# Kernel tuning notes

Hardware: AMD Instinct MI355X
Metric: run time of the kernel (lower is better)

## Reference

```python
import jax, jax.numpy as jnp
import numpy as np

WINDOW_SIZE = 11
CHANNELS = 3
SIGMA = 1.5


def _gaussian_window():
    # 1D gaussian, normalized, then outer product -> [C,1,K,K] depthwise kernel
    x = np.arange(WINDOW_SIZE) - WINDOW_SIZE // 2
    g = np.exp(-(x.astype(np.float32) ** 2) / (2.0 * SIGMA ** 2))
    g = g / g.sum()
    w2d = np.outer(g, g).astype(np.float32)
    w = np.broadcast_to(w2d[None, None], (CHANNELS, 1, WINDOW_SIZE, WINDOW_SIZE))
    return jnp.asarray(np.ascontiguousarray(w))


def _dwconv(x, w):
    # depthwise conv, SAME padding (pad = K//2), NCHW / OIHW layout
    pad = WINDOW_SIZE // 2
    return jax.lax.conv_general_dilated(
        x, w,
        window_strides=(1, 1),
        padding=[(pad, pad), (pad, pad)],
        dimension_numbers=("NCHW", "OIHW", "NCHW"),
        feature_group_count=CHANNELS,
    )


def setup_inputs() -> dict:
    key = jax.random.key(0)
    k1, k2 = jax.random.split(key)
    shape = (32, 3, 512, 512)
    img1 = jax.random.normal(k1, shape, dtype=jnp.float32)
    img2 = jax.random.normal(k2, shape, dtype=jnp.float32)
    return {"img1": img1, "img2": img2}


def reference(img1, img2):
    w = _gaussian_window().astype(img1.dtype)
    x1 = (img1 + 1.0) * 0.5
    x2 = (img2 + 1.0) * 0.5

    mu1 = _dwconv(x1, w)
    mu2 = _dwconv(x2, w)
    mu1_sq = mu1 * mu1
    mu2_sq = mu2 * mu2
    mu1_mu2 = mu1 * mu2

    sigma1_sq = _dwconv(x1 * x1, w) - mu1_sq
    sigma2_sq = _dwconv(x2 * x2, w) - mu2_sq
    sigma12 = _dwconv(x1 * x2, w) - mu1_mu2

    C1 = 0.01 ** 2
    C2 = 0.03 ** 2
    ssim_map = ((2.0 * mu1_mu2 + C1) * (2.0 * sigma12 + C2)) / (
        (mu1_sq + mu2_sq + C1) * (sigma1_sq + sigma2_sq + C2)
    )
    return 1.0 - jnp.mean(ssim_map)
```

## Files before the change

kernel.cpp:

```cpp
#include <hip/hip_runtime.h>
#include <cmath>

#define KW    11
#define PADW  5
#define BX    64
#define BY    32
#define TR    (BY + 2*PADW)
#define HST   68
#define IMG   512
#define NPIX  25165824.0

struct GaussW { float g[6]; };

__global__ __launch_bounds__(256, 2)
void ssim_main(const float* __restrict__ img1, const float* __restrict__ img2,
               double* __restrict__ acc, GaussW gw) {
  __shared__ float hb[5][TR][HST];
  __shared__ float red[4];

  const int tid = threadIdx.x;
  const int x0 = (blockIdx.x & 7) * BX;
  const int y0 = (blockIdx.x >> 3) * BY;
  const size_t plane = (size_t)blockIdx.y * (IMG * IMG);
  const float* base1 = img1 + plane;
  const float* base2 = img2 + plane;

  for (int t = tid; t < TR * 8; t += 256) {
    const int r = t >> 3;
    const int g = t & 7;
    const int gy = y0 - PADW + r;
    const int xb = x0 + 8 * g - 8;
    const bool rowok = ((unsigned)gy < (unsigned)IMG);

    float a[24], b[24];
    #pragma unroll
    for (int i = 0; i < 6; i++) {
      const int cb = xb + 4 * i;
      if (rowok && ((unsigned)cb < (unsigned)IMG)) {
        const float4 v1 = *(const float4*)(base1 + (size_t)gy * IMG + cb);
        const float4 v2 = *(const float4*)(base2 + (size_t)gy * IMG + cb);
        a[4*i+0] = fmaf(v1.x, 0.5f, 0.5f);  b[4*i+0] = fmaf(v2.x, 0.5f, 0.5f);
        a[4*i+1] = fmaf(v1.y, 0.5f, 0.5f);  b[4*i+1] = fmaf(v2.y, 0.5f, 0.5f);
        a[4*i+2] = fmaf(v1.z, 0.5f, 0.5f);  b[4*i+2] = fmaf(v2.z, 0.5f, 0.5f);
        a[4*i+3] = fmaf(v1.w, 0.5f, 0.5f);  b[4*i+3] = fmaf(v2.w, 0.5f, 0.5f);
      } else {
        a[4*i+0] = 0.f; a[4*i+1] = 0.f; a[4*i+2] = 0.f; a[4*i+3] = 0.f;
        b[4*i+0] = 0.f; b[4*i+1] = 0.f; b[4*i+2] = 0.f; b[4*i+3] = 0.f;
      }
    }

    float p11[18], p22[18], p12[18];
    #pragma unroll
    for (int i = 0; i < 18; i++) {
      const float u = a[i + 3], v = b[i + 3];
      p11[i] = u * u; p22[i] = v * v; p12[i] = u * v;
    }

    float c0[8], c1[8], c2[8], c3[8], c4[8];
    #pragma unroll
    for (int j = 0; j < 8; j++) { c0[j]=0.f; c1[j]=0.f; c2[j]=0.f; c3[j]=0.f; c4[j]=0.f; }
    #pragma unroll
    for (int k = 0; k < KW; k++) {
      const float gk = gw.g[(k < 6) ? k : 10 - k];
      #pragma unroll
      for (int j = 0; j < 8; j++) {
        c0[j] = fmaf(gk, a[j + 3 + k], c0[j]);
        c1[j] = fmaf(gk, b[j + 3 + k], c1[j]);
        c2[j] = fmaf(gk, p11[j + k], c2[j]);
        c3[j] = fmaf(gk, p22[j + k], c3[j]);
        c4[j] = fmaf(gk, p12[j + k], c4[j]);
      }
    }

    const int col = 8 * g;
    *(float4*)&hb[0][r][col]     = make_float4(c0[0], c0[1], c0[2], c0[3]);
    *(float4*)&hb[0][r][col + 4] = make_float4(c0[4], c0[5], c0[6], c0[7]);
    *(float4*)&hb[1][r][col]     = make_float4(c1[0], c1[1], c1[2], c1[3]);
    *(float4*)&hb[1][r][col + 4] = make_float4(c1[4], c1[5], c1[6], c1[7]);
    *(float4*)&hb[2][r][col]     = make_float4(c2[0], c2[1], c2[2], c2[3]);
    *(float4*)&hb[2][r][col + 4] = make_float4(c2[4], c2[5], c2[6], c2[7]);
    *(float4*)&hb[3][r][col]     = make_float4(c3[0], c3[1], c3[2], c3[3]);
    *(float4*)&hb[3][r][col + 4] = make_float4(c3[4], c3[5], c3[6], c3[7]);
    *(float4*)&hb[4][r][col]     = make_float4(c4[0], c4[1], c4[2], c4[3]);
    *(float4*)&hb[4][r][col + 4] = make_float4(c4[4], c4[5], c4[6], c4[7]);
  }

  __syncthreads();

  const int w = tid >> 6;
  const int c = tid & 63;
  const int ys = 8 * w;

  const float C1 = (float)(0.01 * 0.01);
  const float C2 = (float)(0.03 * 0.03);

  float win[5][11];
  #pragma unroll
  for (int t = 0; t < 10; t++) {
    #pragma unroll
    for (int q = 0; q < 5; q++) win[q][t] = hb[q][ys + t][c];
  }

  float accs = 0.f;
  #pragma unroll
  for (int i = 0; i < 8; i++) {
    #pragma unroll
    for (int q = 0; q < 5; q++) win[q][(10 + i) % 11] = hb[q][ys + 10 + i][c];

    float vb[5];
    #pragma unroll
    for (int q = 0; q < 5; q++) {
      float s = 0.f;
      #pragma unroll
      for (int k = 0; k < KW; k++) {
        const float gk = gw.g[(k < 6) ? k : 10 - k];
        s = fmaf(gk, win[q][(i + k) % 11], s);
      }
      vb[q] = s;
    }

    const float mu1 = vb[0], mu2 = vb[1];
    const float m11 = mu1 * mu1, m22 = mu2 * mu2, m12 = mu1 * mu2;
    const float s11 = vb[2] - m11;
    const float s22 = vb[3] - m22;
    const float s12 = vb[4] - m12;
    const float num = fmaf(2.f, m12, C1) * fmaf(2.f, s12, C2);
    const float den = (m11 + m22 + C1) * (s11 + s22 + C2);
    accs += num / den;
  }

  float s = accs;
  #pragma unroll
  for (int m = 32; m >= 1; m >>= 1) s += __shfl_xor(s, m, 64);
  if (c == 0) red[w] = s;
  __syncthreads();
  if (tid == 0) {
    const double bs = (double)red[0] + (double)red[1] + (double)red[2] + (double)red[3];
    atomicAdd(acc, bs);
  }
}

__global__ void ssim_fin(const double* __restrict__ acc, float* __restrict__ out) {
  out[0] = 1.0f - (float)(acc[0] * (1.0 / NPIX));
}

extern "C" void kernel_launch(void* const* d_in, const int* in_sizes, int n_in,
                              void* d_out, int out_size, void* d_ws, size_t ws_size,
                              hipStream_t stream) {
  const float* img1 = (const float*)d_in[0];
  const float* img2 = (const float*)d_in[1];
  float* out = (float*)d_out;
  double* acc = (double*)d_ws;

  hipMemsetAsync(acc, 0, sizeof(double), stream);

  GaussW gw;
  {
    double e[11], s = 0.0;
    for (int i = 0; i < 11; i++) {
      const double x = (double)(i - 5);
      e[i] = exp(-(x * x) / (2.0 * 1.5 * 1.5));
      s += e[i];
    }
    for (int i = 0; i < 6; i++) gw.g[i] = (float)(e[i] / s);
  }

  dim3 grid(128, 96);
  ssim_main<<<grid, 256, 0, stream>>>(img1, img2, acc, gw);
  ssim_fin<<<1, 1, 0, stream>>>(acc, out);
}
```

Baseline: 365.0 us.

## Halve tile height, raise occupancy, and skip bounds checks on interior tiles

Tile height drops from 32 to 16 rows, so the grid doubles and each thread's vertical pass handles 4 output rows instead of 8. Launch bounds now ask for 4 blocks per CU, and the LDS buffer shrinks. Interior tiles take a specialised horizontal pass with no per-load bounds checks. The trade-off is a larger halo overhead: 26 staged rows per 16 outputs instead of 42 per 32, which means more redundant loads and horizontal FMAs per output pixel.

```diff
diff --git a/kernel.cpp b/kernel.cpp
--- a/kernel.cpp
+++ b/kernel.cpp
@@ -4,7 +4,7 @@
 #define KW    11
 #define PADW  5
 #define BX    64
-#define BY    32
+#define BY    16
 #define TR    (BY + 2*PADW)
 #define HST   68
 #define IMG   512
@@ -12,40 +12,46 @@
 
 struct GaussW { float g[6]; };
 
-__global__ __launch_bounds__(256, 2)
-void ssim_main(const float* __restrict__ img1, const float* __restrict__ img2,
-               double* __restrict__ acc, GaussW gw) {
-  __shared__ float hb[5][TR][HST];
-  __shared__ float red[4];
-
-  const int tid = threadIdx.x;
-  const int x0 = (blockIdx.x & 7) * BX;
-  const int y0 = (blockIdx.x >> 3) * BY;
-  const size_t plane = (size_t)blockIdx.y * (IMG * IMG);
-  const float* base1 = img1 + plane;
-  const float* base2 = img2 + plane;
-
-  for (int t = tid; t < TR * 8; t += 256) {
-    const int r = t >> 3;
-    const int g = t & 7;
+template<bool CHK>
+__device__ __forceinline__ void hpass(const float* __restrict__ base1,
+                                      const float* __restrict__ base2,
+                                      int x0, int y0, const GaussW& gw,
+                                      float (&hb)[5][TR][HST], int tid) {
+  if (tid < TR * 8) {
+    const int r = tid >> 3;
+    const int g = tid & 7;
     const int gy = y0 - PADW + r;
     const int xb = x0 + 8 * g - 8;
-    const bool rowok = ((unsigned)gy < (unsigned)IMG);
 
     float a[24], b[24];
-    #pragma unroll
-    for (int i = 0; i < 6; i++) {
-      const int cb = xb + 4 * i;
-      if (rowok && ((unsigned)cb < (unsigned)IMG)) {
-        const float4 v1 = *(const float4*)(base1 + (size_t)gy * IMG + cb);
-        const float4 v2 = *(const float4*)(base2 + (size_t)gy * IMG + cb);
+    if (CHK) {
+      const bool rowok = ((unsigned)gy < (unsigned)IMG);
+      #pragma unroll
+      for (int i = 0; i < 6; i++) {
+        const int cb = xb + 4 * i;
+        if (rowok && ((unsigned)cb < (unsigned)IMG)) {
+          const float4 v1 = *(const float4*)(base1 + (size_t)gy * IMG + cb);
+          const float4 v2 = *(const float4*)(base2 + (size_t)gy * IMG + cb);
+          a[4*i+0] = fmaf(v1.x, 0.5f, 0.5f);  b[4*i+0] = fmaf(v2.x, 0.5f, 0.5f);
+          a[4*i+1] = fmaf(v1.y, 0.5f, 0.5f);  b[4*i+1] = fmaf(v2.y, 0.5f, 0.5f);
+          a[4*i+2] = fmaf(v1.z, 0.5f, 0.5f);  b[4*i+2] = fmaf(v2.z, 0.5f, 0.5f);
+          a[4*i+3] = fmaf(v1.w, 0.5f, 0.5f);  b[4*i+3] = fmaf(v2.w, 0.5f, 0.5f);
+        } else {
+          a[4*i+0] = 0.f; a[4*i+1] = 0.f; a[4*i+2] = 0.f; a[4*i+3] = 0.f;
+          b[4*i+0] = 0.f; b[4*i+1] = 0.f; b[4*i+2] = 0.f; b[4*i+3] = 0.f;
+        }
+      }
+    } else {
+      const float* p1 = base1 + (size_t)gy * IMG + xb;
+      const float* p2 = base2 + (size_t)gy * IMG + xb;
+      #pragma unroll
+      for (int i = 0; i < 6; i++) {
+        const float4 v1 = *(const float4*)(p1 + 4 * i);
+        const float4 v2 = *(const float4*)(p2 + 4 * i);
         a[4*i+0] = fmaf(v1.x, 0.5f, 0.5f);  b[4*i+0] = fmaf(v2.x, 0.5f, 0.5f);
         a[4*i+1] = fmaf(v1.y, 0.5f, 0.5f);  b[4*i+1] = fmaf(v2.y, 0.5f, 0.5f);
         a[4*i+2] = fmaf(v1.z, 0.5f, 0.5f);  b[4*i+2] = fmaf(v2.z, 0.5f, 0.5f);
         a[4*i+3] = fmaf(v1.w, 0.5f, 0.5f);  b[4*i+3] = fmaf(v2.w, 0.5f, 0.5f);
-      } else {
-        a[4*i+0] = 0.f; a[4*i+1] = 0.f; a[4*i+2] = 0.f; a[4*i+3] = 0.f;
-        b[4*i+0] = 0.f; b[4*i+1] = 0.f; b[4*i+2] = 0.f; b[4*i+3] = 0.f;
       }
     }
 
@@ -84,12 +90,34 @@
     *(float4*)&hb[4][r][col]     = make_float4(c4[0], c4[1], c4[2], c4[3]);
     *(float4*)&hb[4][r][col + 4] = make_float4(c4[4], c4[5], c4[6], c4[7]);
   }
+}
+
+__global__ __launch_bounds__(256, 4)
+void ssim_main(const float* __restrict__ img1, const float* __restrict__ img2,
+               double* __restrict__ acc, GaussW gw) {
+  __shared__ float hb[5][TR][HST];
+  __shared__ float red[4];
+
+  const int tid = threadIdx.x;
+  const int tx = blockIdx.x & 7;
+  const int ty = blockIdx.x >> 3;
+  const int x0 = tx * BX;
+  const int y0 = ty * BY;
+  const size_t plane = (size_t)blockIdx.y * (IMG * IMG);
+  const float* base1 = img1 + plane;
+  const float* base2 = img2 + plane;
+
+  if (tx >= 1 && tx <= 6 && ty >= 1 && ty <= 30) {
+    hpass<false>(base1, base2, x0, y0, gw, hb, tid);
+  } else {
+    hpass<true>(base1, base2, x0, y0, gw, hb, tid);
+  }
 
   __syncthreads();
 
   const int w = tid >> 6;
   const int c = tid & 63;
-  const int ys = 8 * w;
+  const int ys = 4 * w;
 
   const float C1 = (float)(0.01 * 0.01);
   const float C2 = (float)(0.03 * 0.03);
@@ -103,7 +131,7 @@
 
   float accs = 0.f;
   #pragma unroll
-  for (int i = 0; i < 8; i++) {
+  for (int i = 0; i < 4; i++) {
     #pragma unroll
     for (int q = 0; q < 5; q++) win[q][(10 + i) % 11] = hb[q][ys + 10 + i][c];
 
@@ -165,7 +193,7 @@
     for (int i = 0; i < 6; i++) gw.g[i] = (float)(e[i] / s);
   }
 
-  dim3 grid(128, 96);
+  dim3 grid(256, 96);
   ssim_main<<<grid, 256, 0, stream>>>(img1, img2, acc, gw);
   ssim_fin<<<1, 1, 0, stream>>>(acc, out);
 }
```

After: 924.2 us. 2.53x slower.

## Compute separable Gaussian convolutions as fp16 MFMA banded-matrix products

Applied to the files above, without the earlier changes.

Both the horizontal and vertical 11-tap blur passes are recast as multiplications by banded Toeplitz matrices built in registers, executed with 16x16x16 fp16 MFMA instructions instead of scalar FMA loops. The intermediate row-blurred planes are stored in shared memory as fp16 in a transposed layout, which halves LDS footprint, and the division is replaced by a hardware reciprocal. The aim is to move the convolution arithmetic onto the matrix cores. In exchange, inputs, squared products and intermediates lose precision in fp16, which risks cancellation error in the variance terms (E[x^2]-mu^2).

```diff
diff --git a/kernel.cpp b/kernel.cpp
--- a/kernel.cpp
+++ b/kernel.cpp
@@ -1,138 +1,149 @@
 #include <hip/hip_runtime.h>
 #include <cmath>
 
-#define KW    11
-#define PADW  5
-#define BX    64
-#define BY    32
-#define TR    (BY + 2*PADW)
-#define HST   68
 #define IMG   512
 #define NPIX  25165824.0
+#define RST   48
+#define QSTR  (64 * RST)
 
-struct GaussW { float g[6]; };
+typedef _Float16 f16x4 __attribute__((ext_vector_type(4)));
+typedef float    f32x4 __attribute__((ext_vector_type(4)));
+
+__device__ __forceinline__ _Float16 bandval(int t, float invS) {
+  if (t < 0 || t > 10) return (_Float16)0.f;
+  const float d = (float)(t - 5);
+  return (_Float16)(__expf(-d * d * (1.0f / 4.5f)) * invS);
+}
 
 __global__ __launch_bounds__(256, 2)
 void ssim_main(const float* __restrict__ img1, const float* __restrict__ img2,
-               double* __restrict__ acc, GaussW gw) {
-  __shared__ float hb[5][TR][HST];
+               double* __restrict__ acc, float invS) {
+  __shared__ _Float16 hb[5 * QSTR];
   __shared__ float red[4];
 
-  const int tid = threadIdx.x;
-  const int x0 = (blockIdx.x & 7) * BX;
-  const int y0 = (blockIdx.x >> 3) * BY;
+  const int tid  = threadIdx.x;
+  const int w    = tid >> 6;
+  const int ln15 = tid & 15;
+  const int lg   = (tid & 63) >> 4;
+
+  const int tx = blockIdx.x & 7;
+  const int ty = blockIdx.x >> 3;
+  const int xg = tx * 64;
+  const int yg = ty * 32;
   const size_t plane = (size_t)blockIdx.y * (IMG * IMG);
-  const float* base1 = img1 + plane;
-  const float* base2 = img2 + plane;
+  const float* b1 = img1 + plane;
+  const float* b2 = img2 + plane;
 
-  for (int t = tid; t < TR * 8; t += 256) {
-    const int r = t >> 3;
-    const int g = t & 7;
-    const int gy = y0 - PADW + r;
-    const int xb = x0 + 8 * g - 8;
-    const bool rowok = ((unsigned)gy < (unsigned)IMG);
+  f16x4 bH0, bH1, bV0, bV1;
+  #pragma unroll
+  for (int i = 0; i < 4; i++) {
+    const int kb = 4 * lg + i - ln15;
+    bH0[i] = bandval(kb - 3,  invS);
+    bH1[i] = bandval(kb + 13, invS);
+    bV0[i] = bandval(kb,      invS);
+    bV1[i] = bandval(kb + 16, invS);
+  }
 
-    float a[24], b[24];
+  const bool interior = (tx >= 1 && tx <= 6 && ty >= 1 && ty <= 14);
+  const int x0 = 16 * w;
+
+  for (int rt = 0; rt < 3; rt++) {
+    const int r0 = 16 * rt;
+    const int grow = yg - 5 + r0 + ln15;
+    f32x4 d0 = {0.f,0.f,0.f,0.f}, d1 = d0, d2 = d0, d3 = d0, d4 = d0;
     #pragma unroll
-    for (int i = 0; i < 6; i++) {
-      const int cb = xb + 4 * i;
-      if (rowok && ((unsigned)cb < (unsigned)IMG)) {
-        const float4 v1 = *(const float4*)(base1 + (size_t)gy * IMG + cb);
-        const float4 v2 = *(const float4*)(base2 + (size_t)gy * IMG + cb);
-        a[4*i+0] = fmaf(v1.x, 0.5f, 0.5f);  b[4*i+0] = fmaf(v2.x, 0.5f, 0.5f);
-        a[4*i+1] = fmaf(v1.y, 0.5f, 0.5f);  b[4*i+1] = fmaf(v2.y, 0.5f, 0.5f);
-        a[4*i+2] = fmaf(v1.z, 0.5f, 0.5f);  b[4*i+2] = fmaf(v2.z, 0.5f, 0.5f);
-        a[4*i+3] = fmaf(v1.w, 0.5f, 0.5f);  b[4*i+3] = fmaf(v2.w, 0.5f, 0.5f);
+    for (int h = 0; h < 2; h++) {
+      const int gxb = xg + x0 - 8 + 16 * h + 4 * lg;
+      float av[4], bv[4];
+      if (interior) {
+        const f32x4 v1 = *(const f32x4*)(b1 + (size_t)grow * IMG + gxb);
+        const f32x4 v2 = *(const f32x4*)(b2 + (size_t)grow * IMG + gxb);
+        #pragma unroll
+        for (int e = 0; e < 4; e++) { av[e] = v1[e]; bv[e] = v2[e]; }
       } else {
-        a[4*i+0] = 0.f; a[4*i+1] = 0.f; a[4*i+2] = 0.f; a[4*i+3] = 0.f;
-        b[4*i+0] = 0.f; b[4*i+1] = 0.f; b[4*i+2] = 0.f; b[4*i+3] = 0.f;
+        const int  crow = grow < 0 ? 0 : (grow > IMG - 1 ? IMG - 1 : grow);
+        const bool rok  = (unsigned)grow < (unsigned)IMG;
+        #pragma unroll
+        for (int e = 0; e < 4; e++) {
+          const int  xi  = gxb + e;
+          const int  cxi = xi < 0 ? 0 : (xi > IMG - 1 ? IMG - 1 : xi);
+          const bool ok  = rok && ((unsigned)xi < (unsigned)IMG);
+          av[e] = ok ? b1[(size_t)crow * IMG + cxi] : 0.f;
+          bv[e] = ok ? b2[(size_t)crow * IMG + cxi] : 0.f;
+        }
       }
+      f16x4 fa, fb, f11, f22, f12;
+      #pragma unroll
+      for (int e = 0; e < 4; e++) {
+        const float ax = fmaf(av[e], 0.5f, 0.5f);
+        const float bx = fmaf(bv[e], 0.5f, 0.5f);
+        fa[e]  = (_Float16)ax;
+        fb[e]  = (_Float16)bx;
+        f11[e] = (_Float16)(ax * ax);
+        f22[e] = (_Float16)(bx * bx);
+        f12[e] = (_Float16)(ax * bx);
+      }
+      const f16x4 bh = h ? bH1 : bH0;
+      d0 = __builtin_amdgcn_mfma_f32_16x16x16f16(fa,  bh, d0, 0, 0, 0);
+      d1 = __builtin_amdgcn_mfma_f32_16x16x16f16(fb,  bh, d1, 0, 0, 0);
+      d2 = __builtin_amdgcn_mfma_f32_16x16x16f16(f11, bh, d2, 0, 0, 0);
+      d3 = __builtin_amdgcn_mfma_f32_16x16x16f16(f22, bh, d3, 0, 0, 0);
+      d4 = __builtin_amdgcn_mfma_f32_16x16x16f16(f12, bh, d4, 0, 0, 0);
     }
-
-    float p11[18], p22[18], p12[18];
+    const int wbase = (x0 + ln15) * RST + r0 + 4 * lg;
+    f16x4 s;
     #pragma unroll
-    for (int i = 0; i < 18; i++) {
-      const float u = a[i + 3], v = b[i + 3];
-      p11[i] = u * u; p22[i] = v * v; p12[i] = u * v;
-    }
-
-    float c0[8], c1[8], c2[8], c3[8], c4[8];
+    for (int e = 0; e < 4; e++) s[e] = (_Float16)d0[e];
+    *(f16x4*)&hb[0 * QSTR + wbase] = s;
     #pragma unroll
-    for (int j = 0; j < 8; j++) { c0[j]=0.f; c1[j]=0.f; c2[j]=0.f; c3[j]=0.f; c4[j]=0.f; }
+    for (int e = 0; e < 4; e++) s[e] = (_Float16)d1[e];
+    *(f16x4*)&hb[1 * QSTR + wbase] = s;
     #pragma unroll
-    for (int k = 0; k < KW; k++) {
-      const float gk = gw.g[(k < 6) ? k : 10 - k];
-      #pragma unroll
-      for (int j = 0; j < 8; j++) {
-        c0[j] = fmaf(gk, a[j + 3 + k], c0[j]);
-        c1[j] = fmaf(gk, b[j + 3 + k], c1[j]);
-        c2[j] = fmaf(gk, p11[j + k], c2[j]);
-        c3[j] = fmaf(gk, p22[j + k], c3[j]);
-        c4[j] = fmaf(gk, p12[j + k], c4[j]);
-      }
-    }
-
-    const int col = 8 * g;
-    *(float4*)&hb[0][r][col]     = make_float4(c0[0], c0[1], c0[2], c0[3]);
-    *(float4*)&hb[0][r][col + 4] = make_float4(c0[4], c0[5], c0[6], c0[7]);
-    *(float4*)&hb[1][r][col]     = make_float4(c1[0], c1[1], c1[2], c1[3]);
-    *(float4*)&hb[1][r][col + 4] = make_float4(c1[4], c1[5], c1[6], c1[7]);
-    *(float4*)&hb[2][r][col]     = make_float4(c2[0], c2[1], c2[2], c2[3]);
-    *(float4*)&hb[2][r][col + 4] = make_float4(c2[4], c2[5], c2[6], c2[7]);
-    *(float4*)&hb[3][r][col]     = make_float4(c3[0], c3[1], c3[2], c3[3]);
-    *(float4*)&hb[3][r][col + 4] = make_float4(c3[4], c3[5], c3[6], c3[7]);
-    *(float4*)&hb[4][r][col]     = make_float4(c4[0], c4[1], c4[2], c4[3]);
-    *(float4*)&hb[4][r][col + 4] = make_float4(c4[4], c4[5], c4[6], c4[7]);
+    for (int e = 0; e < 4; e++) s[e] = (_Float16)d2[e];
+    *(f16x4*)&hb[2 * QSTR + wbase] = s;
+    #pragma unroll
+    for (int e = 0; e < 4; e++) s[e] = (_Float16)d3[e];
+    *(f16x4*)&hb[3 * QSTR + wbase] = s;
+    #pragma unroll
+    for (int e = 0; e < 4; e++) s[e] = (_Float16)d4[e];
+    *(f16x4*)&hb[4 * QSTR + wbase] = s;
   }
 
   __syncthreads();
 
-  const int w = tid >> 6;
-  const int c = tid & 63;
-  const int ys = 8 * w;
-
-  const float C1 = (float)(0.01 * 0.01);
-  const float C2 = (float)(0.03 * 0.03);
-
-  float win[5][11];
+  const float C1 = 1.0e-4f;
+  const float C2 = 9.0e-4f;
+  float ssum = 0.f;
+  const int rbase = (x0 + ln15) * RST + 4 * lg;
   #pragma unroll
-  for (int t = 0; t < 10; t++) {
+  for (int yt = 0; yt < 2; yt++) {
+    f32x4 e0 = {0.f,0.f,0.f,0.f}, e1 = e0, e2 = e0, e3 = e0, e4 = e0;
     #pragma unroll
-    for (int q = 0; q < 5; q++) win[q][t] = hb[q][ys + t][c];
+    for (int h = 0; h < 2; h++) {
+      const int off = rbase + 16 * yt + 16 * h;
+      const f16x4 bv = h ? bV1 : bV0;
+      e0 = __builtin_amdgcn_mfma_f32_16x16x16f16(bv, *(const f16x4*)&hb[0 * QSTR + off], e0, 0, 0, 0);
+      e1 = __builtin_amdgcn_mfma_f32_16x16x16f16(bv, *(const f16x4*)&hb[1 * QSTR + off], e1, 0, 0, 0);
+      e2 = __builtin_amdgcn_mfma_f32_16x16x16f16(bv, *(const f16x4*)&hb[2 * QSTR + off], e2, 0, 0, 0);
+      e3 = __builtin_amdgcn_mfma_f32_16x16x16f16(bv, *(const f16x4*)&hb[3 * QSTR + off], e3, 0, 0, 0);
+      e4 = __builtin_amdgcn_mfma_f32_16x16x16f16(bv, *(const f16x4*)&hb[4 * QSTR + off], e4, 0, 0, 0);
+    }
+    #pragma unroll
+    for (int el = 0; el < 4; el++) {
+      const float mu1 = e0[el], mu2 = e1[el];
+      const float m11 = mu1 * mu1, m22 = mu2 * mu2, m12 = mu1 * mu2;
+      const float s11 = e2[el] - m11;
+      const float s22 = e3[el] - m22;
+      const float s12 = e4[el] - m12;
+      const float num = fmaf(2.f, m12, C1) * fmaf(2.f, s12, C2);
+      const float den = (m11 + m22 + C1) * (s11 + s22 + C2);
+      ssum += num * __builtin_amdgcn_rcpf(den);
+    }
   }
 
-  float accs = 0.f;
   #pragma unroll
-  for (int i = 0; i < 8; i++) {
-    #pragma unroll
-    for (int q = 0; q < 5; q++) win[q][(10 + i) % 11] = hb[q][ys + 10 + i][c];
-
-    float vb[5];
-    #pragma unroll
-    for (int q = 0; q < 5; q++) {
-      float s = 0.f;
-      #pragma unroll
-      for (int k = 0; k < KW; k++) {
-        const float gk = gw.g[(k < 6) ? k : 10 - k];
-        s = fmaf(gk, win[q][(i + k) % 11], s);
-      }
-      vb[q] = s;
-    }
-
-    const float mu1 = vb[0], mu2 = vb[1];
-    const float m11 = mu1 * mu1, m22 = mu2 * mu2, m12 = mu1 * mu2;
-    const float s11 = vb[2] - m11;
-    const float s22 = vb[3] - m22;
-    const float s12 = vb[4] - m12;
-    const float num = fmaf(2.f, m12, C1) * fmaf(2.f, s12, C2);
-    const float den = (m11 + m22 + C1) * (s11 + s22 + C2);
-    accs += num / den;
-  }
-
-  float s = accs;
-  #pragma unroll
-  for (int m = 32; m >= 1; m >>= 1) s += __shfl_xor(s, m, 64);
-  if (c == 0) red[w] = s;
+  for (int m = 32; m >= 1; m >>= 1) ssum += __shfl_xor(ssum, m, 64);
+  if ((tid & 63) == 0) red[w] = ssum;
   __syncthreads();
   if (tid == 0) {
     const double bs = (double)red[0] + (double)red[1] + (double)red[2] + (double)red[3];
@@ -154,18 +165,14 @@
 
   hipMemsetAsync(acc, 0, sizeof(double), stream);
 
-  GaussW gw;
-  {
-    double e[11], s = 0.0;
-    for (int i = 0; i < 11; i++) {
-      const double x = (double)(i - 5);
-      e[i] = exp(-(x * x) / (2.0 * 1.5 * 1.5));
-      s += e[i];
-    }
-    for (int i = 0; i < 6; i++) gw.g[i] = (float)(e[i] / s);
+  double S = 0.0;
+  for (int i = 0; i < 11; i++) {
+    const double x = (double)(i - 5);
+    S += exp(-(x * x) / (2.0 * 1.5 * 1.5));
   }
+  const float invS = (float)(1.0 / S);
 
   dim3 grid(128, 96);
-  ssim_main<<<grid, 256, 0, stream>>>(img1, img2, acc, gw);
+  ssim_main<<<grid, 256, 0, stream>>>(img1, img2, acc, invS);
   ssim_fin<<<1, 1, 0, stream>>>(acc, out);
 }
```

Result: slower. 396.4 us (+8.6%).
